# Performance work log

Measured on AMD Instinct MI355X. Metric: run time of the kernel, lower is better.

## Reference

```python
import jax, jax.numpy as jnp
import numpy as np

TOPK = 2


def setup_inputs() -> dict:
    key = jax.random.key(0)
    k1, k2 = jax.random.split(key)
    B, N, D, E, C = 4, 2048, 2048, 8, 512
    token_inputs = jax.random.normal(k1, (B, N, D), dtype=jnp.float32)
    # bottleneck_in.weight.t() stacked over experts: [E, D, C]; scaled like a real init
    bottleneck_weights = jax.random.normal(k2, (E, D, C), dtype=jnp.float32) * 0.02
    return {
        "token_inputs": token_inputs,
        "bottleneck_weights": bottleneck_weights,
        "expert_capacity": 640,
    }


def _routing(router_probs, expert_capacity, topk):
    # router_probs: [B, N, E]
    B, N, E = router_probs.shape
    _, expert_indices = jax.lax.top_k(router_probs, topk)      # [B, N, topk]
    idx = jnp.transpose(expert_indices, (0, 2, 1)).reshape(B, topk * N)
    expert_mask = jax.nn.one_hot(idx, E, dtype=jnp.int32)       # [B, topk*N, E]
    token_priority = jnp.cumsum(expert_mask, axis=1) * expert_mask - 1
    token_priority = token_priority.reshape(B, topk, N, E)
    token_priority = jnp.transpose(token_priority, (0, 2, 1, 3))  # [B, N, topk, E]
    token_priority = jnp.max(token_priority, axis=2)              # [B, N, E]
    # one-hot over capacity; negative (-1) and >= capacity priorities map to all-zero rows
    cap_range = jnp.arange(expert_capacity, dtype=jnp.int32)
    dispatch = (token_priority[..., None] == cap_range).astype(jnp.float32)  # [B,N,E,C]
    combine = router_probs[..., None] * dispatch                            # [B,N,E,C]
    return dispatch, combine


def reference(token_inputs, bottleneck_weights, expert_capacity):
    # activation_cache: [B, N, E, Cb]
    activation_cache = jnp.einsum("bnd,edc->bnec", token_inputs, bottleneck_weights)
    router_logits = jnp.sqrt(jnp.sum(activation_cache * activation_cache, axis=-1))  # [B,N,E]
    router_probs = jax.nn.softmax(router_logits, axis=-1)
    dispatch, combine = _routing(router_probs, expert_capacity, TOPK)
    return jnp.stack([dispatch, combine], axis=0)  # [2, B, N, E, capacity]
```

## Files before the change

kernel.cpp:

```cpp
#include <hip/hip_runtime.h>
#include <math.h>

constexpr int Bb = 4, Nn = 2048, Dd = 2048, Ee = 8, Cbn = 512;
constexpr int Mm = Bb * Nn;

typedef _Float16 half8 __attribute__((ext_vector_type(8)));
typedef float floatx16 __attribute__((ext_vector_type(16)));

#define GLL16(g, l)                                                     \
  __builtin_amdgcn_global_load_lds(                                     \
      (const __attribute__((address_space(1))) void*)(g),               \
      (__attribute__((address_space(3))) void*)(l), 16, 0, 0)

__global__ __launch_bounds__(256) void transpose_w(const float* __restrict__ W,
                                                   _Float16* __restrict__ WThi,
                                                   _Float16* __restrict__ WTlo) {
  const int kt = blockIdx.x;
  const int ct = blockIdx.y;
  const int e = blockIdx.z;
  __shared__ _Float16 thi[64][72];
  __shared__ _Float16 tlo[64][72];
  const int tx = threadIdx.x & 15, ty = threadIdx.x >> 4;
  const float* src = W + ((size_t)(e * 2048 + kt * 64)) * 512 + ct * 64;
#pragma unroll
  for (int p = 0; p < 4; ++p) {
    int kk = ty + p * 16;
    float4 v = *(const float4*)(src + (size_t)kk * 512 + tx * 4);
    _Float16 h;
    h = (_Float16)v.x; thi[tx * 4 + 0][kk] = h; tlo[tx * 4 + 0][kk] = (_Float16)(v.x - (float)h);
    h = (_Float16)v.y; thi[tx * 4 + 1][kk] = h; tlo[tx * 4 + 1][kk] = (_Float16)(v.y - (float)h);
    h = (_Float16)v.z; thi[tx * 4 + 2][kk] = h; tlo[tx * 4 + 2][kk] = (_Float16)(v.z - (float)h);
    h = (_Float16)v.w; thi[tx * 4 + 3][kk] = h; tlo[tx * 4 + 3][kk] = (_Float16)(v.w - (float)h);
  }
  __syncthreads();
  const int rr = threadIdx.x >> 3;
  const int ch = threadIdx.x & 7;
  _Float16* dh = WThi + ((size_t)(e * 512 + ct * 64)) * 2048 + kt * 64;
  _Float16* dl = WTlo + ((size_t)(e * 512 + ct * 64)) * 2048 + kt * 64;
#pragma unroll
  for (int p = 0; p < 2; ++p) {
    int cc = rr + p * 32;
    *(half8*)(dh + (size_t)cc * 2048 + ch * 8) = *(const half8*)(&thi[cc][ch * 8]);
    *(half8*)(dl + (size_t)cc * 2048 + ch * 8) = *(const half8*)(&tlo[cc][ch * 8]);
  }
}

__global__ __launch_bounds__(256) void gemm_mfma(const float* __restrict__ X,
                                                 const _Float16* __restrict__ WThi,
                                                 const _Float16* __restrict__ WTlo,
                                                 float* __restrict__ partial) {
  const int bid = blockIdx.x;
  const int st = bid >> 8;
  const int stm = st & 3;
  const int stn = st >> 2;
  const int li = bid & 255;
  const int mtile = stm * 16 + (li >> 4);
  const int ntile = stn * 16 + (li & 15);

  const int tid = threadIdx.x;
  const int wave = tid >> 6, lane = tid & 63;
  const int wm = wave >> 1, wn = wave & 1;
  const int h = lane >> 5;

  __shared__ __align__(16) char lds[32768];
  char* ldsA = lds;
  char* ldsBhi = lds + 16384;
  char* ldsBlo = lds + 24576;

  const int lrA = lane >> 3;
  const int cposA = lane & 7;
  const int cgA = cposA ^ lrA;
  const float* xg[4];
  int ldsAoff[4];
#pragma unroll
  for (int q = 0; q < 4; ++q) {
    const int row = wave * 32 + q * 8 + lrA;
    xg[q] = X + (size_t)(mtile * 128 + row) * 2048 + cgA * 4;
    ldsAoff[q] = (wave * 32 + q * 8) * 128;
  }

  const int lrB = lane >> 2;
  const int cposB = lane & 3;
  const int cgB = cposB ^ ((lrB >> 1) & 3);
  const int rB0s = wave * 32 + lrB;
  const int rB1s = rB0s + 16;
  const _Float16* wh0 = WThi + (size_t)(ntile * 128 + rB0s) * 2048 + cgB * 8;
  const _Float16* wh1 = WThi + (size_t)(ntile * 128 + rB1s) * 2048 + cgB * 8;
  const _Float16* wl0 = WTlo + (size_t)(ntile * 128 + rB0s) * 2048 + cgB * 8;
  const _Float16* wl1 = WTlo + (size_t)(ntile * 128 + rB1s) * 2048 + cgB * 8;
  const int lqB0 = wave * 2048;
  const int lqB1 = lqB0 + 1024;

  const int keyA = lane & 7;
  const int rowA0 = wm * 64 + (lane & 31);
  const int rowA1 = rowA0 + 32;
  int oAf0[2][2], oAf1[2][2];
#pragma unroll
  for (int s = 0; s < 2; ++s)
#pragma unroll
    for (int c = 0; c < 2; ++c) {
      const int g = s * 4 + h * 2 + c;
      oAf0[s][c] = rowA0 * 128 + ((g ^ keyA) << 4);
      oAf1[s][c] = rowA1 * 128 + ((g ^ keyA) << 4);
    }

  const int rB0 = wn * 64 + (lane & 31);
  const int rB1 = rB0 + 32;
  auto foffB = [&](int r, int s) {
    return r * 64 + (((s * 2 + h) ^ ((r >> 1) & 3)) << 4);
  };
  const int oB0[2] = {foffB(rB0, 0), foffB(rB0, 1)};
  const int oB1[2] = {foffB(rB1, 0), foffB(rB1, 1)};

  floatx16 acc00 = {}, acc01 = {}, acc10 = {}, acc11 = {};

  auto cvtA = [](const char* p0, const char* p1, half8& ah, half8& al) {
    float4 f0 = *(const float4*)p0;
    float4 f1 = *(const float4*)p1;
    float xf[8] = {f0.x, f0.y, f0.z, f0.w, f1.x, f1.y, f1.z, f1.w};
#pragma unroll
    for (int j = 0; j < 8; ++j) {
      _Float16 hv = (_Float16)xf[j];
      ah[j] = hv;
      al[j] = (_Float16)(xf[j] - (float)hv);
    }
  };

  for (int kt = 0; kt < 64; ++kt) {
    const int k0 = kt * 32;
#pragma unroll
    for (int q = 0; q < 4; ++q) GLL16(xg[q] + k0, ldsA + ldsAoff[q]);
    GLL16(wh0 + k0, ldsBhi + lqB0);
    GLL16(wh1 + k0, ldsBhi + lqB1);
    GLL16(wl0 + k0, ldsBlo + lqB0);
    GLL16(wl1 + k0, ldsBlo + lqB1);
    __syncthreads();
#pragma unroll
    for (int s = 0; s < 2; ++s) {
      half8 ah0, al0, ah1, al1;
      cvtA(ldsA + oAf0[s][0], ldsA + oAf0[s][1], ah0, al0);
      cvtA(ldsA + oAf1[s][0], ldsA + oAf1[s][1], ah1, al1);
      half8 bh0 = *(const half8*)(ldsBhi + oB0[s]);
      half8 bh1 = *(const half8*)(ldsBhi + oB1[s]);
      half8 bl0 = *(const half8*)(ldsBlo + oB0[s]);
      half8 bl1 = *(const half8*)(ldsBlo + oB1[s]);
      acc00 = __builtin_amdgcn_mfma_f32_32x32x16_f16(ah0, bh0, acc00, 0, 0, 0);
      acc00 = __builtin_amdgcn_mfma_f32_32x32x16_f16(ah0, bl0, acc00, 0, 0, 0);
      acc00 = __builtin_amdgcn_mfma_f32_32x32x16_f16(al0, bh0, acc00, 0, 0, 0);
      acc01 = __builtin_amdgcn_mfma_f32_32x32x16_f16(ah0, bh1, acc01, 0, 0, 0);
      acc01 = __builtin_amdgcn_mfma_f32_32x32x16_f16(ah0, bl1, acc01, 0, 0, 0);
      acc01 = __builtin_amdgcn_mfma_f32_32x32x16_f16(al0, bh1, acc01, 0, 0, 0);
      acc10 = __builtin_amdgcn_mfma_f32_32x32x16_f16(ah1, bh0, acc10, 0, 0, 0);
      acc10 = __builtin_amdgcn_mfma_f32_32x32x16_f16(ah1, bl0, acc10, 0, 0, 0);
      acc10 = __builtin_amdgcn_mfma_f32_32x32x16_f16(al1, bh0, acc10, 0, 0, 0);
      acc11 = __builtin_amdgcn_mfma_f32_32x32x16_f16(ah1, bh1, acc11, 0, 0, 0);
      acc11 = __builtin_amdgcn_mfma_f32_32x32x16_f16(ah1, bl1, acc11, 0, 0, 0);
      acc11 = __builtin_amdgcn_mfma_f32_32x32x16_f16(al1, bh1, acc11, 0, 0, 0);
    }
    __syncthreads();
  }

  float myv = 0.f;
#pragma unroll
  for (int i = 0; i < 2; ++i) {
    const floatx16& c0 = i ? acc10 : acc00;
    const floatx16& c1 = i ? acc11 : acc01;
#pragma unroll
    for (int reg = 0; reg < 16; ++reg) {
      float v = c0[reg] * c0[reg] + c1[reg] * c1[reg];
#pragma unroll
      for (int m = 1; m <= 16; m <<= 1) v += __shfl_xor(v, m, 64);
      if ((lane & 31) == i * 16 + reg) myv = v;
    }
  }
  {
    const int i = (lane & 31) >> 4;
    const int reg = lane & 15;
    const int row = i * 32 + (reg & 3) + 8 * (reg >> 2) + 4 * h;
    const int token = mtile * 128 + wm * 64 + row;
    const int slice = ntile * 2 + wn;
    partial[(size_t)token * 64 + slice] = myv;
  }
}

__global__ void route_kernel(const float* __restrict__ partial,
                             int* __restrict__ idx1, int* __restrict__ idx2,
                             float* __restrict__ p1, float* __restrict__ p2) {
  int t = blockIdx.x * blockDim.x + threadIdx.x;
  if (t >= Mm) return;
  float l[Ee];
  float mx = -1e30f;
#pragma unroll
  for (int e = 0; e < Ee; ++e) {
    float s = 0.f;
#pragma unroll
    for (int u = 0; u < 8; ++u) s += partial[(size_t)t * 64 + e * 8 + u];
    l[e] = sqrtf(s);
    mx = fmaxf(mx, l[e]);
  }
  float p[Ee];
  float s = 0.f;
#pragma unroll
  for (int e = 0; e < Ee; ++e) {
    p[e] = expf(l[e] - mx);
    s += p[e];
  }
  float inv = 1.f / s;
  int i1 = 0;
  float b1 = l[0];
#pragma unroll
  for (int e = 1; e < Ee; ++e)
    if (l[e] > b1) { b1 = l[e]; i1 = e; }
  int i2 = -1;
  float b2 = -1e30f;
#pragma unroll
  for (int e = 0; e < Ee; ++e)
    if (e != i1 && l[e] > b2) { b2 = l[e]; i2 = e; }
  idx1[t] = i1;
  idx2[t] = i2;
  p1[t] = p[i1] * inv;
  p2[t] = p[i2] * inv;
}

__global__ void scan_kernel(const int* __restrict__ idx1,
                            const int* __restrict__ idx2,
                            int* __restrict__ prios) {
  const int b = blockIdx.x;
  const int tid = threadIdx.x;
  __shared__ int cnts[256][8];
  int cnt[8] = {0, 0, 0, 0, 0, 0, 0, 0};
  int eloc[16];
  const int base_p = tid * 16;
#pragma unroll
  for (int i = 0; i < 16; ++i) {
    int p = base_p + i;
    int k = p >> 11;
    int n = p & (Nn - 1);
    int e = (k == 0 ? idx1 : idx2)[b * Nn + n];
    eloc[i] = e;
    cnt[e]++;
  }
#pragma unroll
  for (int e = 0; e < 8; ++e) cnts[tid][e] = cnt[e];
  __syncthreads();
  if (tid < 8) {
    int run = 0;
    for (int i = 0; i < 256; ++i) {
      int v = cnts[i][tid];
      cnts[i][tid] = run;
      run += v;
    }
  }
  __syncthreads();
  int base[8];
#pragma unroll
  for (int e = 0; e < 8; ++e) base[e] = cnts[tid][e];
#pragma unroll
  for (int i = 0; i < 16; ++i) {
    int e = eloc[i];
    prios[b * 2 * Nn + base_p + i] = base[e]++;
  }
}

__global__ void zero_kernel(float4* __restrict__ out, int n4) {
  int i = blockIdx.x * blockDim.x + threadIdx.x;
  if (i < n4) out[i] = make_float4(0.f, 0.f, 0.f, 0.f);
}

__global__ void scatter_kernel(const int* __restrict__ idx1,
                               const int* __restrict__ idx2,
                               const float* __restrict__ p1,
                               const float* __restrict__ p2,
                               const int* __restrict__ prios,
                               float* __restrict__ out, int cap) {
  int t = blockIdx.x * blockDim.x + threadIdx.x;
  if (t >= Mm) return;
  int b = t >> 11;
  int n = t & (Nn - 1);
  size_t disp = (size_t)t * Ee * cap;
  size_t comb = disp + (size_t)Mm * Ee * cap;
  {
    int e = idx1[t];
    int p = prios[b * 2 * Nn + n];
    if (p < cap) {
      out[disp + (size_t)e * cap + p] = 1.f;
      out[comb + (size_t)e * cap + p] = p1[t];
    }
  }
  {
    int e = idx2[t];
    int p = prios[b * 2 * Nn + Nn + n];
    if (p < cap) {
      out[disp + (size_t)e * cap + p] = 1.f;
      out[comb + (size_t)e * cap + p] = p2[t];
    }
  }
}

extern "C" void kernel_launch(void* const* d_in, const int* in_sizes, int n_in,
                              void* d_out, int out_size, void* d_ws, size_t ws_size,
                              hipStream_t stream) {
  const float* X = (const float*)d_in[0];
  const float* W = (const float*)d_in[1];
  float* out = (float*)d_out;
  const int cap = out_size / (2 * Bb * Nn * Ee);

  char* ws = (char*)d_ws;
  _Float16* WThi = (_Float16*)ws;
  _Float16* WTlo = (_Float16*)(ws + 16777216ull);
  float* partial = (float*)(ws + 33554432ull);
  int* idx1 = (int*)(ws + 35651584ull);
  int* idx2 = idx1 + Mm;
  float* p1 = (float*)(idx2 + Mm);
  float* p2 = p1 + Mm;
  int* prios = (int*)(p2 + Mm);

  transpose_w<<<dim3(32, 8, 8), 256, 0, stream>>>(W, WThi, WTlo);
  gemm_mfma<<<2048, 256, 0, stream>>>(X, WThi, WTlo, partial);
  route_kernel<<<Mm / 256, 256, 0, stream>>>(partial, idx1, idx2, p1, p2);
  scan_kernel<<<Bb, 256, 0, stream>>>(idx1, idx2, prios);
  const int n4 = out_size / 4;
  zero_kernel<<<(n4 + 255) / 256, 256, 0, stream>>>((float4*)out, n4);
  scatter_kernel<<<Mm / 256, 256, 0, stream>>>(idx1, idx2, p1, p2, prios, out, cap);
}
```

Baseline: 808.9 us.

## Fuse routing into scan and write output rows densely instead of zero+scatter

Routing (softmax, top-2) now runs inside the per-batch scan kernel and keeps expert indices in shared memory, removing one launch and a global round trip. The separate zero-fill and scatter kernels become one kernel that writes each token's full dispatch and combine rows with float4 stores, placing the one-hot values inline. This avoids writing the large output twice. The cost is that routing now runs on only 4 blocks, which serialises work that used to spread across many blocks.

Measured after the change: 824.4 us. About the same (+1.9%).

```diff
diff --git a/kernel.cpp b/kernel.cpp
--- a/kernel.cpp
+++ b/kernel.cpp
@@ -183,60 +183,64 @@
   }
 }
 
-__global__ void route_kernel(const float* __restrict__ partial,
-                             int* __restrict__ idx1, int* __restrict__ idx2,
-                             float* __restrict__ p1, float* __restrict__ p2) {
-  int t = blockIdx.x * blockDim.x + threadIdx.x;
-  if (t >= Mm) return;
-  float l[Ee];
-  float mx = -1e30f;
-#pragma unroll
-  for (int e = 0; e < Ee; ++e) {
-    float s = 0.f;
-#pragma unroll
-    for (int u = 0; u < 8; ++u) s += partial[(size_t)t * 64 + e * 8 + u];
-    l[e] = sqrtf(s);
-    mx = fmaxf(mx, l[e]);
-  }
-  float p[Ee];
-  float s = 0.f;
-#pragma unroll
-  for (int e = 0; e < Ee; ++e) {
-    p[e] = expf(l[e] - mx);
-    s += p[e];
-  }
-  float inv = 1.f / s;
-  int i1 = 0;
-  float b1 = l[0];
-#pragma unroll
-  for (int e = 1; e < Ee; ++e)
-    if (l[e] > b1) { b1 = l[e]; i1 = e; }
-  int i2 = -1;
-  float b2 = -1e30f;
-#pragma unroll
-  for (int e = 0; e < Ee; ++e)
-    if (e != i1 && l[e] > b2) { b2 = l[e]; i2 = e; }
-  idx1[t] = i1;
-  idx2[t] = i2;
-  p1[t] = p[i1] * inv;
-  p2[t] = p[i2] * inv;
-}
-
-__global__ void scan_kernel(const int* __restrict__ idx1,
-                            const int* __restrict__ idx2,
-                            int* __restrict__ prios) {
+__global__ __launch_bounds__(256) void scan_route(const float* __restrict__ partial,
+                                                  int* __restrict__ ig,
+                                                  float* __restrict__ p1g,
+                                                  float* __restrict__ p2g,
+                                                  int* __restrict__ prios) {
   const int b = blockIdx.x;
   const int tid = threadIdx.x;
+  __shared__ unsigned char sI1[Nn];
+  __shared__ unsigned char sI2[Nn];
   __shared__ int cnts[256][8];
+
+  for (int i = 0; i < 8; ++i) {
+    const int tl = i * 256 + tid;
+    const int t = b * Nn + tl;
+    float l[Ee];
+    float mx = -1e30f;
+#pragma unroll
+    for (int e = 0; e < Ee; ++e) {
+      float s = 0.f;
+#pragma unroll
+      for (int u = 0; u < 8; ++u) s += partial[(size_t)t * 64 + e * 8 + u];
+      l[e] = sqrtf(s);
+      mx = fmaxf(mx, l[e]);
+    }
+    float sum = 0.f, pe[Ee];
+#pragma unroll
+    for (int e = 0; e < Ee; ++e) {
+      pe[e] = expf(l[e] - mx);
+      sum += pe[e];
+    }
+    float inv = 1.f / sum;
+    int i1 = 0;
+    float b1 = l[0];
+#pragma unroll
+    for (int e = 1; e < Ee; ++e)
+      if (l[e] > b1) { b1 = l[e]; i1 = e; }
+    int i2 = -1;
+    float b2 = -1e30f;
+#pragma unroll
+    for (int e = 0; e < Ee; ++e)
+      if (e != i1 && l[e] > b2) { b2 = l[e]; i2 = e; }
+    sI1[tl] = (unsigned char)i1;
+    sI2[tl] = (unsigned char)i2;
+    ig[t] = i1 | (i2 << 8);
+    p1g[t] = pe[i1] * inv;
+    p2g[t] = pe[i2] * inv;
+  }
+  __syncthreads();
+
   int cnt[8] = {0, 0, 0, 0, 0, 0, 0, 0};
   int eloc[16];
   const int base_p = tid * 16;
 #pragma unroll
   for (int i = 0; i < 16; ++i) {
-    int p = base_p + i;
-    int k = p >> 11;
-    int n = p & (Nn - 1);
-    int e = (k == 0 ? idx1 : idx2)[b * Nn + n];
+    int pp = base_p + i;
+    int k = pp >> 11;
+    int n = pp & (Nn - 1);
+    int e = k == 0 ? (int)sI1[n] : (int)sI2[n];
     eloc[i] = e;
     cnt[e]++;
   }
@@ -262,38 +266,38 @@
   }
 }
 
-__global__ void zero_kernel(float4* __restrict__ out, int n4) {
-  int i = blockIdx.x * blockDim.x + threadIdx.x;
-  if (i < n4) out[i] = make_float4(0.f, 0.f, 0.f, 0.f);
-}
-
-__global__ void scatter_kernel(const int* __restrict__ idx1,
-                               const int* __restrict__ idx2,
-                               const float* __restrict__ p1,
-                               const float* __restrict__ p2,
-                               const int* __restrict__ prios,
-                               float* __restrict__ out, int cap) {
-  int t = blockIdx.x * blockDim.x + threadIdx.x;
-  if (t >= Mm) return;
-  int b = t >> 11;
-  int n = t & (Nn - 1);
-  size_t disp = (size_t)t * Ee * cap;
-  size_t comb = disp + (size_t)Mm * Ee * cap;
-  {
-    int e = idx1[t];
-    int p = prios[b * 2 * Nn + n];
-    if (p < cap) {
-      out[disp + (size_t)e * cap + p] = 1.f;
-      out[comb + (size_t)e * cap + p] = p1[t];
-    }
-  }
-  {
-    int e = idx2[t];
-    int p = prios[b * 2 * Nn + Nn + n];
-    if (p < cap) {
-      out[disp + (size_t)e * cap + p] = 1.f;
-      out[comb + (size_t)e * cap + p] = p2[t];
-    }
+__global__ __launch_bounds__(256) void out_kernel(const int* __restrict__ ig,
+                                                  const float* __restrict__ p1g,
+                                                  const float* __restrict__ p2g,
+                                                  const int* __restrict__ prios,
+                                                  float* __restrict__ out, int cap) {
+  const int t = blockIdx.x;
+  const int tid = threadIdx.x;
+  const int b = t >> 11, n = t & (Nn - 1);
+  const int pair = ig[t];
+  const int e1 = pair & 0xff, e2 = (pair >> 8) & 0xff;
+  const int q1 = prios[b * 2 * Nn + n];
+  const int q2 = prios[b * 2 * Nn + Nn + n];
+  const float v1 = p1g[t], v2 = p2g[t];
+  const int g1 = (q1 < cap) ? e1 * cap + q1 : -1;
+  const int g2 = (q2 < cap) ? e2 * cap + q2 : -1;
+  const int row4 = Ee * cap / 4;
+  float4* drow = (float4*)out + (size_t)t * row4;
+  float4* crow = drow + (size_t)Mm * row4;
+  for (int f = tid; f < row4; f += 256) {
+    float4 d = make_float4(0.f, 0.f, 0.f, 0.f);
+    float4 c = make_float4(0.f, 0.f, 0.f, 0.f);
+    const int base = f * 4;
+    if (g1 >= base && g1 < base + 4) {
+      ((float*)&d)[g1 - base] = 1.f;
+      ((float*)&c)[g1 - base] = v1;
+    }
+    if (g2 >= base && g2 < base + 4) {
+      ((float*)&d)[g2 - base] = 1.f;
+      ((float*)&c)[g2 - base] = v2;
+    }
+    drow[f] = d;
+    crow[f] = c;
   }
 }
 
@@ -309,17 +313,13 @@
   _Float16* WThi = (_Float16*)ws;
   _Float16* WTlo = (_Float16*)(ws + 16777216ull);
   float* partial = (float*)(ws + 33554432ull);
-  int* idx1 = (int*)(ws + 35651584ull);
-  int* idx2 = idx1 + Mm;
-  float* p1 = (float*)(idx2 + Mm);
-  float* p2 = p1 + Mm;
-  int* prios = (int*)(p2 + Mm);
+  int* ig = (int*)(ws + 35651584ull);
+  float* p1g = (float*)(ig + Mm);
+  float* p2g = p1g + Mm;
+  int* prios = (int*)(p2g + Mm);
 
   transpose_w<<<dim3(32, 8, 8), 256, 0, stream>>>(W, WThi, WTlo);
   gemm_mfma<<<2048, 256, 0, stream>>>(X, WThi, WTlo, partial);
-  route_kernel<<<Mm / 256, 256, 0, stream>>>(partial, idx1, idx2, p1, p2);
-  scan_kernel<<<Bb, 256, 0, stream>>>(idx1, idx2, prios);
-  const int n4 = out_size / 4;
-  zero_kernel<<<(n4 + 255) / 256, 256, 0, stream>>>((float4*)out, n4);
-  scatter_kernel<<<Mm / 256, 256, 0, stream>>>(idx1, idx2, p1, p2, prios, out, cap);
-}
+  scan_route<<<Bb, 256, 0, stream>>>(partial, ig, p1g, p2g, prios);
+  out_kernel<<<Mm, 256, 0, stream>>>(ig, p1g, p2g, prios, out, cap);
+}
```

## Double-buffer LDS tiles with K-step 16 to overlap global loads with MFMA

Applied to the files above, without the earlier changes.

Splits the 32 KB single LDS buffer into two 16 KB buffers and halves the K tile to 16, so the next tile's global_load_lds is issued right after the barrier while MFMAs run on the current buffer. It removes the second barrier per iteration and changes the swizzle layouts to fit the narrower tiles. In exchange it doubles the iteration count and the number of barriers. Each load is smaller and there is less work per barrier, and it relies on the barrier to wait for the async LDS loads to land.

Result: slower. 883.2 us (+9.2%).

```diff
diff --git a/kernel.cpp b/kernel.cpp
--- a/kernel.cpp
+++ b/kernel.cpp
@@ -62,57 +62,46 @@
   const int wm = wave >> 1, wn = wave & 1;
   const int h = lane >> 5;
 
-  __shared__ __align__(16) char lds[32768];
-  char* ldsA = lds;
-  char* ldsBhi = lds + 16384;
-  char* ldsBlo = lds + 24576;
-
-  const int lrA = lane >> 3;
-  const int cposA = lane & 7;
-  const int cgA = cposA ^ lrA;
-  const float* xg[4];
-  int ldsAoff[4];
-#pragma unroll
-  for (int q = 0; q < 4; ++q) {
-    const int row = wave * 32 + q * 8 + lrA;
-    xg[q] = X + (size_t)(mtile * 128 + row) * 2048 + cgA * 4;
-    ldsAoff[q] = (wave * 32 + q * 8) * 128;
-  }
-
-  const int lrB = lane >> 2;
-  const int cposB = lane & 3;
-  const int cgB = cposB ^ ((lrB >> 1) & 3);
-  const int rB0s = wave * 32 + lrB;
-  const int rB1s = rB0s + 16;
-  const _Float16* wh0 = WThi + (size_t)(ntile * 128 + rB0s) * 2048 + cgB * 8;
-  const _Float16* wh1 = WThi + (size_t)(ntile * 128 + rB1s) * 2048 + cgB * 8;
-  const _Float16* wl0 = WTlo + (size_t)(ntile * 128 + rB0s) * 2048 + cgB * 8;
-  const _Float16* wl1 = WTlo + (size_t)(ntile * 128 + rB1s) * 2048 + cgB * 8;
-  const int lqB0 = wave * 2048;
-  const int lqB1 = lqB0 + 1024;
-
-  const int keyA = lane & 7;
+  __shared__ __align__(16) char lds[2][16384];
+
+  const float* xgA[2];
+  int ldsAoff[2];
+#pragma unroll
+  for (int q = 0; q < 2; ++q) {
+    const int row = wave * 32 + q * 16 + (lane >> 2);
+    const int cg = (lane & 3) ^ ((row >> 1) & 3);
+    xgA[q] = X + (size_t)(mtile * 128 + row) * 2048 + cg * 4;
+    ldsAoff[q] = wave * 2048 + q * 1024;
+  }
+  const int rowBd = wave * 32 + (lane >> 1);
+  const int cgB = (lane & 1) ^ ((rowBd >> 2) & 1);
+  const _Float16* wgh = WThi + (size_t)(ntile * 128 + rowBd) * 2048 + cgB * 8;
+  const _Float16* wgl = WTlo + (size_t)(ntile * 128 + rowBd) * 2048 + cgB * 8;
+  const int ldsBoff = wave * 1024;
+
   const int rowA0 = wm * 64 + (lane & 31);
   const int rowA1 = rowA0 + 32;
-  int oAf0[2][2], oAf1[2][2];
-#pragma unroll
-  for (int s = 0; s < 2; ++s)
-#pragma unroll
-    for (int c = 0; c < 2; ++c) {
-      const int g = s * 4 + h * 2 + c;
-      oAf0[s][c] = rowA0 * 128 + ((g ^ keyA) << 4);
-      oAf1[s][c] = rowA1 * 128 + ((g ^ keyA) << 4);
-    }
-
-  const int rB0 = wn * 64 + (lane & 31);
-  const int rB1 = rB0 + 32;
-  auto foffB = [&](int r, int s) {
-    return r * 64 + (((s * 2 + h) ^ ((r >> 1) & 3)) << 4);
+  int oA0[2], oA1[2];
+#pragma unroll
+  for (int c = 0; c < 2; ++c) {
+    oA0[c] = rowA0 * 64 + (((h * 2 + c) ^ ((rowA0 >> 1) & 3)) << 4);
+    oA1[c] = rowA1 * 64 + (((h * 2 + c) ^ ((rowA1 >> 1) & 3)) << 4);
+  }
+  const int rowB0 = wn * 64 + (lane & 31);
+  const int rowB1 = rowB0 + 32;
+  const int oB0 = rowB0 * 32 + ((h ^ ((rowB0 >> 2) & 1)) << 4);
+  const int oB1 = rowB1 * 32 + ((h ^ ((rowB1 >> 2) & 1)) << 4);
+
+  floatx16 acc00 = {}, acc01 = {}, acc10 = {}, acc11 = {};
+
+  auto issue = [&](int kt, int buf) {
+    char* L = lds[buf];
+    const int kA = kt * 16;
+#pragma unroll
+    for (int q = 0; q < 2; ++q) GLL16(xgA[q] + kA, L + ldsAoff[q]);
+    GLL16(wgh + kA, L + 8192 + ldsBoff);
+    GLL16(wgl + kA, L + 12288 + ldsBoff);
   };
-  const int oB0[2] = {foffB(rB0, 0), foffB(rB0, 1)};
-  const int oB1[2] = {foffB(rB1, 0), foffB(rB1, 1)};
-
-  floatx16 acc00 = {}, acc01 = {}, acc10 = {}, acc11 = {};
 
   auto cvtA = [](const char* p0, const char* p1, half8& ah, half8& al) {
     float4 f0 = *(const float4*)p0;
@@ -126,38 +115,34 @@
     }
   };
 
-  for (int kt = 0; kt < 64; ++kt) {
-    const int k0 = kt * 32;
-#pragma unroll
-    for (int q = 0; q < 4; ++q) GLL16(xg[q] + k0, ldsA + ldsAoff[q]);
-    GLL16(wh0 + k0, ldsBhi + lqB0);
-    GLL16(wh1 + k0, ldsBhi + lqB1);
-    GLL16(wl0 + k0, ldsBlo + lqB0);
-    GLL16(wl1 + k0, ldsBlo + lqB1);
+  issue(0, 0);
+  int q = 0;
+  for (int kt = 0; kt < 128; ++kt) {
     __syncthreads();
-#pragma unroll
-    for (int s = 0; s < 2; ++s) {
-      half8 ah0, al0, ah1, al1;
-      cvtA(ldsA + oAf0[s][0], ldsA + oAf0[s][1], ah0, al0);
-      cvtA(ldsA + oAf1[s][0], ldsA + oAf1[s][1], ah1, al1);
-      half8 bh0 = *(const half8*)(ldsBhi + oB0[s]);
-      half8 bh1 = *(const half8*)(ldsBhi + oB1[s]);
-      half8 bl0 = *(const half8*)(ldsBlo + oB0[s]);
-      half8 bl1 = *(const half8*)(ldsBlo + oB1[s]);
-      acc00 = __builtin_amdgcn_mfma_f32_32x32x16_f16(ah0, bh0, acc00, 0, 0, 0);
-      acc00 = __builtin_amdgcn_mfma_f32_32x32x16_f16(ah0, bl0, acc00, 0, 0, 0);
-      acc00 = __builtin_amdgcn_mfma_f32_32x32x16_f16(al0, bh0, acc00, 0, 0, 0);
-      acc01 = __builtin_amdgcn_mfma_f32_32x32x16_f16(ah0, bh1, acc01, 0, 0, 0);
-      acc01 = __builtin_amdgcn_mfma_f32_32x32x16_f16(ah0, bl1, acc01, 0, 0, 0);
-      acc01 = __builtin_amdgcn_mfma_f32_32x32x16_f16(al0, bh1, acc01, 0, 0, 0);
-      acc10 = __builtin_amdgcn_mfma_f32_32x32x16_f16(ah1, bh0, acc10, 0, 0, 0);
-      acc10 = __builtin_amdgcn_mfma_f32_32x32x16_f16(ah1, bl0, acc10, 0, 0, 0);
-      acc10 = __builtin_amdgcn_mfma_f32_32x32x16_f16(al1, bh0, acc10, 0, 0, 0);
-      acc11 = __builtin_amdgcn_mfma_f32_32x32x16_f16(ah1, bh1, acc11, 0, 0, 0);
-      acc11 = __builtin_amdgcn_mfma_f32_32x32x16_f16(ah1, bl1, acc11, 0, 0, 0);
-      acc11 = __builtin_amdgcn_mfma_f32_32x32x16_f16(al1, bh1, acc11, 0, 0, 0);
-    }
-    __syncthreads();
+    if (kt < 127) issue(kt + 1, q ^ 1);
+    const char* A = lds[q];
+    const char* Bhi = A + 8192;
+    const char* Blo = A + 12288;
+    half8 ah0, al0, ah1, al1;
+    cvtA(A + oA0[0], A + oA0[1], ah0, al0);
+    cvtA(A + oA1[0], A + oA1[1], ah1, al1);
+    half8 bh0 = *(const half8*)(Bhi + oB0);
+    half8 bh1 = *(const half8*)(Bhi + oB1);
+    half8 bl0 = *(const half8*)(Blo + oB0);
+    half8 bl1 = *(const half8*)(Blo + oB1);
+    acc00 = __builtin_amdgcn_mfma_f32_32x32x16_f16(ah0, bh0, acc00, 0, 0, 0);
+    acc00 = __builtin_amdgcn_mfma_f32_32x32x16_f16(ah0, bl0, acc00, 0, 0, 0);
+    acc00 = __builtin_amdgcn_mfma_f32_32x32x16_f16(al0, bh0, acc00, 0, 0, 0);
+    acc01 = __builtin_amdgcn_mfma_f32_32x32x16_f16(ah0, bh1, acc01, 0, 0, 0);
+    acc01 = __builtin_amdgcn_mfma_f32_32x32x16_f16(ah0, bl1, acc01, 0, 0, 0);
+    acc01 = __builtin_amdgcn_mfma_f32_32x32x16_f16(al0, bh1, acc01, 0, 0, 0);
+    acc10 = __builtin_amdgcn_mfma_f32_32x32x16_f16(ah1, bh0, acc10, 0, 0, 0);
+    acc10 = __builtin_amdgcn_mfma_f32_32x32x16_f16(ah1, bl0, acc10, 0, 0, 0);
+    acc10 = __builtin_amdgcn_mfma_f32_32x32x16_f16(al1, bh0, acc10, 0, 0, 0);
+    acc11 = __builtin_amdgcn_mfma_f32_32x32x16_f16(ah1, bh1, acc11, 0, 0, 0);
+    acc11 = __builtin_amdgcn_mfma_f32_32x32x16_f16(ah1, bl1, acc11, 0, 0, 0);
+    acc11 = __builtin_amdgcn_mfma_f32_32x32x16_f16(al1, bh1, acc11, 0, 0, 0);
+    q ^= 1;
   }
 
   float myv = 0.f;
```

## Warp-specialize GEMM with producer waves and double-buffered LDS flags

Applied to the files above, without the earlier changes.

The GEMM block gains two producer waves that issue global-to-LDS loads into two 32KB buffers, handing off to the four compute waves through LDS atomic flags instead of __syncthreads. Loads for the next k-tile overlap with MFMA work on the current one. The cost is a 64KB LDS footprint per block, which limits occupancy, plus spin-wait overhead. There is also a risk around waitcnt and flag ordering, since the consumer waves never wait on the loads themselves.

Result: slower. 880.1 us (+8.8%).

```diff
diff --git a/kernel.cpp b/kernel.cpp
--- a/kernel.cpp
+++ b/kernel.cpp
@@ -45,10 +45,10 @@
   }
 }
 
-__global__ __launch_bounds__(256) void gemm_mfma(const float* __restrict__ X,
-                                                 const _Float16* __restrict__ WThi,
-                                                 const _Float16* __restrict__ WTlo,
-                                                 float* __restrict__ partial) {
+__global__ __launch_bounds__(384, 3) void gemm_mfma(const float* __restrict__ X,
+                                                    const _Float16* __restrict__ WThi,
+                                                    const _Float16* __restrict__ WTlo,
+                                                    float* __restrict__ partial) {
   const int bid = blockIdx.x;
   const int st = bid >> 8;
   const int stm = st & 3;
@@ -59,37 +59,47 @@
 
   const int tid = threadIdx.x;
   const int wave = tid >> 6, lane = tid & 63;
+
+  __shared__ __align__(16) char smem[65536];
+  __shared__ int flg[4];
+
+  if (tid < 4) flg[tid] = 0;
+  __syncthreads();
+
+  if (wave >= 4) {
+    const int pb = wave - 4;
+    const int lrA8 = lane >> 3;
+    const int cgA = (lane & 7) ^ lrA8;
+    const float* aBase = X + (size_t)(mtile * 128 + lrA8) * 2048 + cgA * 4;
+    const int lrB16 = lane >> 2;
+    const int cgB = (lane & 3) ^ ((lane >> 3) & 3);
+    const _Float16* bhBase = WThi + (size_t)(ntile * 128 + lrB16) * 2048 + cgB * 8;
+    const _Float16* blBase = WTlo + (size_t)(ntile * 128 + lrB16) * 2048 + cgB * 8;
+    char* L = smem + (pb << 15);
+    for (int f = 0; f < 32; ++f) {
+      if (f > 0) {
+        while (__hip_atomic_load(&flg[2 + pb], __ATOMIC_ACQUIRE,
+                                 __HIP_MEMORY_SCOPE_WORKGROUP) < 4 * f)
+          __builtin_amdgcn_s_sleep(1);
+      }
+      const int k0 = (2 * f + pb) * 32;
+#pragma unroll
+      for (int i = 0; i < 16; ++i)
+        GLL16(aBase + (size_t)(i * 8) * 2048 + k0, L + i * 1024);
+#pragma unroll
+      for (int i = 0; i < 8; ++i) {
+        GLL16(bhBase + (size_t)(i * 16) * 2048 + k0, L + 16384 + i * 1024);
+        GLL16(blBase + (size_t)(i * 16) * 2048 + k0, L + 24576 + i * 1024);
+      }
+      __builtin_amdgcn_s_waitcnt(0x0f70);
+      __hip_atomic_store(&flg[pb], f + 1, __ATOMIC_RELEASE,
+                         __HIP_MEMORY_SCOPE_WORKGROUP);
+    }
+    return;
+  }
+
   const int wm = wave >> 1, wn = wave & 1;
   const int h = lane >> 5;
-
-  __shared__ __align__(16) char lds[32768];
-  char* ldsA = lds;
-  char* ldsBhi = lds + 16384;
-  char* ldsBlo = lds + 24576;
-
-  const int lrA = lane >> 3;
-  const int cposA = lane & 7;
-  const int cgA = cposA ^ lrA;
-  const float* xg[4];
-  int ldsAoff[4];
-#pragma unroll
-  for (int q = 0; q < 4; ++q) {
-    const int row = wave * 32 + q * 8 + lrA;
-    xg[q] = X + (size_t)(mtile * 128 + row) * 2048 + cgA * 4;
-    ldsAoff[q] = (wave * 32 + q * 8) * 128;
-  }
-
-  const int lrB = lane >> 2;
-  const int cposB = lane & 3;
-  const int cgB = cposB ^ ((lrB >> 1) & 3);
-  const int rB0s = wave * 32 + lrB;
-  const int rB1s = rB0s + 16;
-  const _Float16* wh0 = WThi + (size_t)(ntile * 128 + rB0s) * 2048 + cgB * 8;
-  const _Float16* wh1 = WThi + (size_t)(ntile * 128 + rB1s) * 2048 + cgB * 8;
-  const _Float16* wl0 = WTlo + (size_t)(ntile * 128 + rB0s) * 2048 + cgB * 8;
-  const _Float16* wl1 = WTlo + (size_t)(ntile * 128 + rB1s) * 2048 + cgB * 8;
-  const int lqB0 = wave * 2048;
-  const int lqB1 = lqB0 + 1024;
 
   const int keyA = lane & 7;
   const int rowA0 = wm * 64 + (lane & 31);
@@ -103,7 +113,6 @@
       oAf0[s][c] = rowA0 * 128 + ((g ^ keyA) << 4);
       oAf1[s][c] = rowA1 * 128 + ((g ^ keyA) << 4);
     }
-
   const int rB0 = wn * 64 + (lane & 31);
   const int rB1 = rB0 + 32;
   auto foffB = [&](int r, int s) {
@@ -112,8 +121,6 @@
   const int oB0[2] = {foffB(rB0, 0), foffB(rB0, 1)};
   const int oB1[2] = {foffB(rB1, 0), foffB(rB1, 1)};
 
-  floatx16 acc00 = {}, acc01 = {}, acc10 = {}, acc11 = {};
-
   auto cvtA = [](const char* p0, const char* p1, half8& ah, half8& al) {
     float4 f0 = *(const float4*)p0;
     float4 f1 = *(const float4*)p1;
@@ -126,24 +133,25 @@
     }
   };
 
+  floatx16 acc00 = {}, acc01 = {}, acc10 = {}, acc11 = {};
+
   for (int kt = 0; kt < 64; ++kt) {
-    const int k0 = kt * 32;
-#pragma unroll
-    for (int q = 0; q < 4; ++q) GLL16(xg[q] + k0, ldsA + ldsAoff[q]);
-    GLL16(wh0 + k0, ldsBhi + lqB0);
-    GLL16(wh1 + k0, ldsBhi + lqB1);
-    GLL16(wl0 + k0, ldsBlo + lqB0);
-    GLL16(wl1 + k0, ldsBlo + lqB1);
-    __syncthreads();
+    const int b = kt & 1;
+    while (__hip_atomic_load(&flg[b], __ATOMIC_ACQUIRE,
+                             __HIP_MEMORY_SCOPE_WORKGROUP) < (kt >> 1) + 1)
+      __builtin_amdgcn_s_sleep(1);
+    const char* A = smem + (b << 15);
+    const char* Bhi = A + 16384;
+    const char* Blo = A + 24576;
 #pragma unroll
     for (int s = 0; s < 2; ++s) {
       half8 ah0, al0, ah1, al1;
-      cvtA(ldsA + oAf0[s][0], ldsA + oAf0[s][1], ah0, al0);
-      cvtA(ldsA + oAf1[s][0], ldsA + oAf1[s][1], ah1, al1);
-      half8 bh0 = *(const half8*)(ldsBhi + oB0[s]);
-      half8 bh1 = *(const half8*)(ldsBhi + oB1[s]);
-      half8 bl0 = *(const half8*)(ldsBlo + oB0[s]);
-      half8 bl1 = *(const half8*)(ldsBlo + oB1[s]);
+      cvtA(A + oAf0[s][0], A + oAf0[s][1], ah0, al0);
+      cvtA(A + oAf1[s][0], A + oAf1[s][1], ah1, al1);
+      half8 bh0 = *(const half8*)(Bhi + oB0[s]);
+      half8 bh1 = *(const half8*)(Bhi + oB1[s]);
+      half8 bl0 = *(const half8*)(Blo + oB0[s]);
+      half8 bl1 = *(const half8*)(Blo + oB1[s]);
       acc00 = __builtin_amdgcn_mfma_f32_32x32x16_f16(ah0, bh0, acc00, 0, 0, 0);
       acc00 = __builtin_amdgcn_mfma_f32_32x32x16_f16(ah0, bl0, acc00, 0, 0, 0);
       acc00 = __builtin_amdgcn_mfma_f32_32x32x16_f16(al0, bh0, acc00, 0, 0, 0);
@@ -157,7 +165,9 @@
       acc11 = __builtin_amdgcn_mfma_f32_32x32x16_f16(ah1, bl1, acc11, 0, 0, 0);
       acc11 = __builtin_amdgcn_mfma_f32_32x32x16_f16(al1, bh1, acc11, 0, 0, 0);
     }
-    __syncthreads();
+    if (lane == 0)
+      __hip_atomic_fetch_add(&flg[2 + b], 1, __ATOMIC_RELEASE,
+                             __HIP_MEMORY_SCOPE_WORKGROUP);
   }
 
   float myv = 0.f;
@@ -316,7 +326,7 @@
   int* prios = (int*)(p2 + Mm);
 
   transpose_w<<<dim3(32, 8, 8), 256, 0, stream>>>(W, WThi, WTlo);
-  gemm_mfma<<<2048, 256, 0, stream>>>(X, WThi, WTlo, partial);
+  gemm_mfma<<<2048, 384, 0, stream>>>(X, WThi, WTlo, partial);
   route_kernel<<<Mm / 256, 256, 0, stream>>>(partial, idx1, idx2, p1, p2);
   scan_kernel<<<Bb, 256, 0, stream>>>(idx1, idx2, prios);
   const int n4 = out_size / 4;
```
